# Kernel tuning notes

Measured on AMD Instinct MI355X. Metric: run time of the kernel, lower is better.

The kernel has to match this reference:

```python
import jax, jax.numpy as jnp
import numpy as np

DIM = 192
STATE = 64
B = 8
H = 64
W = 64
EPS_LN = 1e-5
EPS_BN = 1e-5


def _layernorm(x, g, b):
    m = jnp.mean(x, axis=-1, keepdims=True)
    v = jnp.mean((x - m) ** 2, axis=-1, keepdims=True)
    return (x - m) / jnp.sqrt(v + EPS_LN) * g + b


def _linear(x, w, b=None):
    # torch Linear convention: w is [out, in]
    y = jnp.einsum('...i,oi->...o', x, w)
    return y if b is None else y + b


def _parallel_scan(A, Bd, xp):
    # A, Bd, xp: [B, L, S]; h_t = A_t*h_{t-1} + Bd_t*xp_t via log-space cumsum
    A_safe = jnp.clip(A, 0.001, 0.999)
    log_A = jnp.log(A_safe + 1e-10)
    log_cum_A = jnp.cumsum(log_A, axis=1)
    log_cum_A_max = jnp.max(log_cum_A, axis=1, keepdims=True)
    cum_A = jnp.exp(log_cum_A - log_cum_A_max)
    BX = Bd * xp
    # prepend zeros, drop last: normalizer uses cumprod up to t-1
    log_pad = jnp.pad(log_cum_A - log_cum_A_max, ((0, 0), (1, 0), (0, 0)))[:, :-1]
    BX_norm = BX * jnp.exp(-log_pad)
    return jnp.cumsum(BX_norm, axis=1) * cum_A


def _ssm(x, ln_g, ln_b, xp_w, xp_b, dt_w, dt_b, A_log, B_w, C_w, Dp, out_w, out_b):
    xn = _layernorm(x, ln_g, ln_b)
    delta = jax.nn.softplus(_linear(xn, dt_w, dt_b)) * 0.01 + 0.0001  # [B,L,S]
    B_t = _linear(xn, B_w)
    C_t = _linear(xn, C_w)
    A = -jnp.exp(A_log)  # [S]
    x_proj = _linear(xn, xp_w, xp_b)
    deltaA = jnp.clip(delta * A, -10.0, -0.0001)
    A_disc = jnp.exp(deltaA)
    B_disc = delta * B_t
    h = _parallel_scan(A_disc, B_disc, x_proj)
    y = C_t * h
    y = jnp.where(jnp.all(jnp.isfinite(y)), y, jnp.zeros_like(y))
    y = _linear(y, out_w, out_b)
    return y + jnp.clip(Dp, -2.0, 2.0) * x


def reference(x, ln1_g, ln1_b, ln2_g, ln2_b, dw_w, bn_g, bn_b, bn_rm, bn_rv,
              ssm_ln_g, ssm_ln_b, xp_w, xp_b, dt_w, dt_b, A_log, B_w, C_w,
              D_param, out_w, out_b, mlp_w1, mlp_b1, mlp_w2, mlp_b2,
              alpha_local, alpha_ssm, alpha_mlp):
    identity = x
    # depthwise 3x3 conv + BatchNorm2d (eval mode, running stats)
    xc = jax.lax.conv_general_dilated(
        x, dw_w, (1, 1), 'SAME', feature_group_count=DIM,
        dimension_numbers=('NCHW', 'OIHW', 'NCHW'))
    scale = (bn_g / jnp.sqrt(bn_rv + EPS_BN))[None, :, None, None]
    x_local = (xc - bn_rm[None, :, None, None]) * scale + bn_b[None, :, None, None]
    # SSM branch on flattened spatial sequence
    x_seq = x.transpose(0, 2, 3, 1).reshape(B, H * W, DIM)
    x_seq = _layernorm(x_seq, ln1_g, ln1_b)
    x_seq = _ssm(x_seq, ssm_ln_g, ssm_ln_b, xp_w, xp_b, dt_w, dt_b, A_log,
                 B_w, C_w, D_param, out_w, out_b)
    x_ssm = x_seq.reshape(B, H, W, DIM).transpose(0, 3, 1, 2)
    xr = identity + alpha_local * x_local + alpha_ssm * x_ssm
    # residual MLP (dropout = identity at inference)
    x_mlp = xr.transpose(0, 2, 3, 1).reshape(B, H * W, DIM)
    x_mlp = _layernorm(x_mlp, ln2_g, ln2_b)
    x_mlp = _linear(jax.nn.gelu(_linear(x_mlp, mlp_w1, mlp_b1), approximate=False),
                    mlp_w2, mlp_b2)
    return xr + alpha_mlp * x_mlp.reshape(B, H, W, DIM).transpose(0, 3, 1, 2)


def setup_inputs() -> dict:
    key = jax.random.key(0)
    ks = jax.random.split(key, 12)
    def nrm(k, shape, s):
        return jax.random.normal(k, shape, jnp.float32) * s
    f32 = jnp.float32
    return {
        'x': jax.random.normal(ks[0], (B, DIM, H, W), f32),
        'ln1_g': jnp.ones(DIM, f32), 'ln1_b': jnp.zeros(DIM, f32),
        'ln2_g': jnp.ones(DIM, f32), 'ln2_b': jnp.zeros(DIM, f32),
        'dw_w': nrm(ks[1], (DIM, 1, 3, 3), 0.2),
        'bn_g': jnp.ones(DIM, f32), 'bn_b': jnp.zeros(DIM, f32),
        'bn_rm': jnp.zeros(DIM, f32), 'bn_rv': jnp.ones(DIM, f32),
        'ssm_ln_g': jnp.ones(DIM, f32), 'ssm_ln_b': jnp.zeros(DIM, f32),
        'xp_w': nrm(ks[2], (STATE, DIM), 0.05), 'xp_b': jnp.zeros(STATE, f32),
        'dt_w': nrm(ks[3], (STATE, DIM), 0.05), 'dt_b': jnp.zeros(STATE, f32),
        'A_log': jnp.log(jax.random.uniform(ks[4], (STATE,), f32) * 0.8 + 0.2),
        'B_w': nrm(ks[5], (STATE, DIM), 0.05),
        'C_w': nrm(ks[6], (STATE, DIM), 0.05),
        'D_param': jnp.zeros(DIM, f32),
        'out_w': nrm(ks[7], (DIM, STATE), 0.05), 'out_b': jnp.zeros(DIM, f32),
        'mlp_w1': nrm(ks[8], (4 * DIM, DIM), 0.03), 'mlp_b1': jnp.zeros(4 * DIM, f32),
        'mlp_w2': nrm(ks[9], (DIM, 4 * DIM), 0.03), 'mlp_b2': jnp.zeros(DIM, f32),
        'alpha_local': jnp.full((1,), 0.5, f32),
        'alpha_ssm': jnp.full((1,), 0.5, f32),
        'alpha_mlp': jnp.full((1,), 0.5, f32),
    }
```

## Files before the change

### kernel.cpp

```cpp
#include <hip/hip_runtime.h>
#include <hip/hip_bf16.h>
#include <math.h>


#define DEV static __device__ __forceinline__

constexpr int Bn = 8, Dm = 192, Ln = 4096, Sn = 64, Hd = 768;

typedef __attribute__((ext_vector_type(8))) short bf16x8;
typedef __attribute__((ext_vector_type(4))) float f32x4;

DEV short f2b(float x) {
  __hip_bfloat16 h = __float2bfloat16(x);
  return *(short*)&h;
}

DEV float b2f(short x) {
  __hip_bfloat16 h = *(__hip_bfloat16*)&x;
  return __bfloat162float(h);
}

__global__ __launch_bounds__(256) void k_prep(
    const float* __restrict__ x, const float* __restrict__ g1, const float* __restrict__ b1,
    const float* __restrict__ g2, const float* __restrict__ b2,
    short* __restrict__ xnb, short* __restrict__ xln1b,
    const float* __restrict__ dt_w, const float* __restrict__ B_w,
    const float* __restrict__ C_w, const float* __restrict__ xp_w,
    const float* __restrict__ out_w, const float* __restrict__ w1,
    const float* __restrict__ w2, short* __restrict__ wb) {
  __shared__ __align__(16) float tile[Dm * 65];
  int tid = threadIdx.x;
  if (blockIdx.y == 8) {
    for (int i = blockIdx.x * 256 + tid; i < 89088; i += 64 * 256) {
      const float4* src;
      if (i < 3072)       src = (const float4*)dt_w + i;
      else if (i < 6144)  src = (const float4*)B_w + (i - 3072);
      else if (i < 9216)  src = (const float4*)C_w + (i - 6144);
      else if (i < 12288) src = (const float4*)xp_w + (i - 9216);
      else if (i < 15360) src = (const float4*)out_w + (i - 12288);
      else if (i < 52224) src = (const float4*)w1 + (i - 15360);
      else                src = (const float4*)w2 + (i - 52224);
      float4 v = *src;
      int o = i * 4;
      wb[o] = f2b(v.x); wb[o + 1] = f2b(v.y); wb[o + 2] = f2b(v.z); wb[o + 3] = f2b(v.w);
    }
    return;
  }
  int b = blockIdx.y, l0 = blockIdx.x * 64;
  const float* xb = x + (size_t)b * Dm * Ln;
  for (int i = tid; i < Dm * 16; i += 256) {
    int d = i >> 4, l4 = (i & 15) << 2;
    float4 v = *(const float4*)&xb[d * Ln + l0 + l4];
    tile[d * 65 + l4]     = v.x; tile[d * 65 + l4 + 1] = v.y;
    tile[d * 65 + l4 + 2] = v.z; tile[d * 65 + l4 + 3] = v.w;
  }
  __syncthreads();
  int pix = tid >> 2, part = tid & 3, c0 = part * 48;
  float v[48];
  float s1 = 0.f, q1 = 0.f;
#pragma unroll
  for (int j = 0; j < 48; j++) {
    float t = tile[(c0 + j) * 65 + pix];
    v[j] = t; s1 += t; q1 += t * t;
  }
  s1 += __shfl_xor(s1, 1); s1 += __shfl_xor(s1, 2);
  q1 += __shfl_xor(q1, 1); q1 += __shfl_xor(q1, 2);
  float m = s1 * (1.f / 192.f);
  float inv = rsqrtf(q1 * (1.f / 192.f) - m * m + 1e-5f);
  float s2 = 0.f, q2 = 0.f;
#pragma unroll
  for (int j = 0; j < 48; j++) {
    float y = (v[j] - m) * inv * g1[c0 + j] + b1[c0 + j];
    v[j] = y; s2 += y; q2 += y * y;
  }
  s2 += __shfl_xor(s2, 1); s2 += __shfl_xor(s2, 2);
  q2 += __shfl_xor(q2, 1); q2 += __shfl_xor(q2, 2);
  float m2 = s2 * (1.f / 192.f);
  float inv2 = rsqrtf(q2 * (1.f / 192.f) - m2 * m2 + 1e-5f);
  size_t base = ((size_t)b * Ln + l0 + pix) * Dm + c0;
#pragma unroll
  for (int j = 0; j < 48; j += 8) {
    int4 yo, no;
    short* yp = (short*)&yo; short* np = (short*)&no;
#pragma unroll
    for (int k = 0; k < 8; k++) {
      float y = v[j + k];
      yp[k] = f2b(y);
      np[k] = f2b((y - m2) * inv2 * g2[c0 + j + k] + b2[c0 + j + k]);
    }
    *(int4*)&xln1b[base + j] = yo;
    *(int4*)&xnb[base + j]   = no;
  }
}

__global__ __launch_bounds__(256) void k_proj(
    const short* __restrict__ xnb, const short* __restrict__ wcat,
    const float* __restrict__ dt_b, const float* __restrict__ xp_b,
    const float* __restrict__ A_log, float* __restrict__ aA, unsigned* __restrict__ bxc,
    float* __restrict__ sums) {
  __shared__ __align__(16) short As[64 * 72];
  __shared__ __align__(16) short Bs[256 * 72];
  int m0 = blockIdx.x * 64, tid = threadIdx.x;
  int lane = tid & 63, l16 = lane & 15, quad = lane >> 4, w = tid >> 6;
  f32x4 acc[16] = {};
  for (int kt = 0; kt < 3; kt++) {
    int kb = kt * 64;
    for (int i = tid; i < 512; i += 256) {
      int row = i >> 3, c8 = (i & 7) * 8;
      *(float4*)&As[row * 72 + c8] = *(const float4*)&xnb[(size_t)(m0 + row) * 192 + kb + c8];
    }
    for (int i = tid; i < 2048; i += 256) {
      int row = i >> 3, c8 = (i & 7) * 8;
      *(float4*)&Bs[row * 72 + c8] = *(const float4*)&wcat[(size_t)row * 192 + kb + c8];
    }
    __syncthreads();
#pragma unroll
    for (int ks = 0; ks < 2; ks++) {
      int ko = ks * 32 + quad * 8;
      bf16x8 a0 = *(const bf16x8*)&As[(w * 16 + l16) * 72 + ko];
#pragma unroll
      for (int nh = 0; nh < 2; nh++) {
        bf16x8 bfr[8];
#pragma unroll
        for (int j = 0; j < 8; j++) bfr[j] = *(const bf16x8*)&Bs[((nh * 8 + j) * 16 + l16) * 72 + ko];
#pragma unroll
        for (int j = 0; j < 8; j++)
          acc[nh * 8 + j] = __builtin_amdgcn_mfma_f32_16x16x32_bf16(a0, bfr[j], acc[nh * 8 + j], 0, 0, 0);
      }
    }
    __syncthreads();
  }
  float* aAs = (float*)Bs;
  float* bxs = aAs + 64 * 65;
  float Av[4], dtbv[4], xpbv[4];
#pragma unroll
  for (int ni = 0; ni < 4; ni++) {
    int s = ni * 16 + l16;
    Av[ni] = -expf(A_log[s]); dtbv[ni] = dt_b[s]; xpbv[ni] = xp_b[s];
  }
#pragma unroll
  for (int r = 0; r < 4; r++) {
    int lm = w * 16 + quad * 4 + r;
    int m = m0 + lm;
#pragma unroll
    for (int ni = 0; ni < 4; ni++) {
      int s = ni * 16 + l16;
      float z = acc[ni][r] + dtbv[ni];
      float sp = (z > 20.f) ? z : log1pf(expf(z));
      float delta = sp * 0.01f + 0.0001f;
      float bt  = acc[ni + 4][r];
      float ct  = acc[ni + 8][r];
      float xpv = acc[ni + 12][r] + xpbv[ni];
      float dA = fminf(fmaxf(delta * Av[ni], -10.f), -0.0001f);
      float Ae = fminf(fmaxf(expf(dA), 0.001f), 0.999f) + 1e-10f;
      short bxh = f2b(delta * bt * xpv);
      aA[(size_t)m * 64 + s] = Ae;
      unsigned pk = (unsigned)(unsigned short)bxh
                  | ((unsigned)(unsigned short)f2b(ct) << 16);
      bxc[(size_t)m * 64 + s] = pk;
      aAs[lm * 65 + s] = Ae;
      bxs[lm * 65 + s] = b2f(bxh);
    }
  }
  __syncthreads();
  int s = tid & 63, seg = tid >> 6, chunk = seg >> 1, sub = seg & 1;
  bool first = ((m0 & 4095) == 0) && (chunk == 0) && (sub == 0);
  float P = 1.f, H = 0.f;
  int base = chunk * 32 + sub * 16;
#pragma unroll
  for (int j = 0; j < 16; j++) {
    float a  = aAs[(base + j) * 65 + s];
    float bx = bxs[(base + j) * 65 + s];
    if (first && j == 0) { P = a; H = bx; }
    else { P *= a; H = a * (H + bx); }
  }
  float* partP = (float*)As;
  float* partH = partP + 256;
  partP[seg * 64 + s] = P; partH[seg * 64 + s] = H;
  __syncthreads();
  if (tid < 128) {
    int c = tid >> 6;
    float p0 = partP[(c * 2) * 64 + s], p1 = partP[(c * 2 + 1) * 64 + s];
    float h0 = partH[(c * 2) * 64 + s], h1 = partH[(c * 2 + 1) * 64 + s];
    int ci = (m0 >> 12) * 128 + ((m0 & 4095) >> 5) + c;
    sums[(ci * 2 + 0) * 64 + s] = p0 * p1;
    sums[(ci * 2 + 1) * 64 + s] = p1 * h0 + h1;
  }
}

__global__ __launch_bounds__(256) void k_conv(
    const float* __restrict__ x, const float* __restrict__ dw,
    const float* __restrict__ bn_g, const float* __restrict__ bn_b,
    const float* __restrict__ bn_rm, const float* __restrict__ bn_rv,
    const float* __restrict__ a_loc, float* __restrict__ xr,
    const float* __restrict__ sums, float* __restrict__ carries) {
  __shared__ __align__(16) float xs[64 * 64];
  int tid = threadIdx.x;
  if (blockIdx.x == 192) {
    float* Pp = xs;
    float* Hp = xs + 256;
    int b = blockIdx.y, s = tid & 63, q = tid >> 6;
    float P = 1.f, H = 0.f;
#pragma unroll 4
    for (int j = 0; j < 32; j++) {
      int ci = b * 128 + q * 32 + j;
      float a = sums[(ci * 2 + 0) * 64 + s];
      float h = sums[(ci * 2 + 1) * 64 + s];
      P *= a; H = a * H + h;
    }
    Pp[q * 64 + s] = P; Hp[q * 64 + s] = H;
    __syncthreads();
    float cur = 0.f;
    for (int qq = 0; qq < q; qq++) cur = Pp[qq * 64 + s] * cur + Hp[qq * 64 + s];
#pragma unroll 4
    for (int j = 0; j < 32; j++) {
      int ci = b * 128 + q * 32 + j;
      carries[ci * 64 + s] = cur;
      float a = sums[(ci * 2 + 0) * 64 + s];
      float h = sums[(ci * 2 + 1) * 64 + s];
      cur = a * cur + h;
    }
    return;
  }
  int d = blockIdx.x, b = blockIdx.y;
  const float* xp = x + ((size_t)b * Dm + d) * Ln;
  for (int i = tid; i < 1024; i += 256) ((float4*)xs)[i] = ((const float4*)xp)[i];
  __syncthreads();
  float w[9];
#pragma unroll
  for (int k = 0; k < 9; k++) w[k] = dw[d * 9 + k];
  float scale = bn_g[d] * rsqrtf(bn_rv[d] + 1e-5f);
  float rm = bn_rm[d], bb = bn_b[d];
  float al = a_loc[0];
  float* xo = xr + ((size_t)b * Dm + d) * Ln;
  for (int i = tid; i < 4096; i += 256) {
    int h = i >> 6, wc = i & 63;
    float acc = 0.f;
#pragma unroll
    for (int kh = 0; kh < 3; kh++) {
      int hh = h + kh - 1;
      if (hh < 0 || hh >= 64) continue;
#pragma unroll
      for (int kw = 0; kw < 3; kw++) {
        int ww2 = wc + kw - 1;
        if (ww2 < 0 || ww2 >= 64) continue;
        acc += xs[hh * 64 + ww2] * w[kh * 3 + kw];
      }
    }
    float xl = (acc - rm) * scale + bb;
    xo[i] = xs[i] + al * xl;
  }
}

__global__ __launch_bounds__(256) void k_out(
    const float* __restrict__ aA, const unsigned* __restrict__ bxc,
    const float* __restrict__ carries,
    const short* __restrict__ owb, const float* __restrict__ out_b,
    const float* __restrict__ Dp, const short* __restrict__ xln1b,
    const float* __restrict__ a_ssm, const float* __restrict__ g2,
    const float* __restrict__ bb2,
    float* __restrict__ xr, short* __restrict__ xn2) {
  __shared__ __align__(16) float smemf[64 * 193];
  short* As = (short*)smemf;
  short* Bs = (short*)smemf + 192 * 72;
  float* tile = smemf;
  int l0g = blockIdx.x * 64, tid = threadIdx.x;
  int lane = tid & 63, l16 = lane & 15, quad = lane >> 4, wv = tid >> 6;
  for (int i = tid; i < 1536; i += 256) {
    int row = i >> 3, c8 = (i & 7) * 8;
    *(float4*)&As[row * 72 + c8] = *(const float4*)&owb[row * 64 + c8];
  }
  int bb = l0g >> 12, c0 = (l0g & 4095) >> 5;
  float xrv[3][4][4];
#pragma unroll
  for (int mi = 0; mi < 3; mi++)
#pragma unroll
    for (int r = 0; r < 4; r++) {
      int d = wv * 48 + mi * 16 + quad * 4 + r;
#pragma unroll
      for (int ni = 0; ni < 4; ni++) {
        int l = l0g + ni * 16 + l16;
        xrv[mi][r][ni] = xr[((size_t)bb * Dm + d) * Ln + (l & 4095)];
      }
    }
  if (wv < 2) {
    int c = c0 + wv, s = lane;
    float h = carries[(bb * 128 + c) * 64 + s];
    const float* ap = aA + (size_t)(l0g + wv * 32) * 64;
    const unsigned* bp = bxc + (size_t)(l0g + wv * 32) * 64;
    int t = 0;
    if (c == 0) {
      unsigned u = bp[s];
      h = b2f((short)(u & 0xFFFF));
      Bs[(wv * 32) * 72 + s] = f2b(b2f((short)(u >> 16)) * h);
      t = 1;
    }
#pragma unroll 4
    for (; t < 32; t++) {
      unsigned u = bp[t * 64 + s];
      float a = ap[t * 64 + s];
      h = a * (h + b2f((short)(u & 0xFFFF)));
      Bs[(wv * 32 + t) * 72 + s] = f2b(b2f((short)(u >> 16)) * h);
    }
  }
  __syncthreads();
  f32x4 acc[3][4] = {};
#pragma unroll
  for (int ks = 0; ks < 2; ks++) {
    int ko = ks * 32 + quad * 8;
    bf16x8 a[3], b[4];
#pragma unroll
    for (int mi = 0; mi < 3; mi++) a[mi] = *(const bf16x8*)&As[(wv * 48 + mi * 16 + l16) * 72 + ko];
#pragma unroll
    for (int ni = 0; ni < 4; ni++) b[ni] = *(const bf16x8*)&Bs[(ni * 16 + l16) * 72 + ko];
#pragma unroll
    for (int mi = 0; mi < 3; mi++)
#pragma unroll
      for (int ni = 0; ni < 4; ni++)
        acc[mi][ni] = __builtin_amdgcn_mfma_f32_16x16x32_bf16(a[mi], b[ni], acc[mi][ni], 0, 0, 0);
  }
  __syncthreads();
  float as_ = a_ssm[0];
#pragma unroll
  for (int mi = 0; mi < 3; mi++)
#pragma unroll
    for (int r = 0; r < 4; r++) {
      int d = wv * 48 + mi * 16 + quad * 4 + r;
      float ob = out_b[d];
      float dc = fminf(fmaxf(Dp[d], -2.f), 2.f);
#pragma unroll
      for (int ni = 0; ni < 4; ni++) {
        int l = l0g + ni * 16 + l16;
        float v = acc[mi][ni][r] + ob;
        if (dc != 0.f) v += dc * b2f(xln1b[(size_t)l * 192 + d]);
        size_t idx = ((size_t)bb * Dm + d) * Ln + (l & 4095);
        float nx = xrv[mi][r][ni] + as_ * v;
        xr[idx] = nx;
        tile[(l & 63) * 193 + d] = nx;
      }
    }
  __syncthreads();
  int pix = tid >> 2, part = tid & 3, c0p = part * 48;
  float vv[48];
  float s1 = 0.f, q1 = 0.f;
#pragma unroll
  for (int j = 0; j < 48; j++) {
    float t = tile[pix * 193 + c0p + j];
    vv[j] = t; s1 += t; q1 += t * t;
  }
  s1 += __shfl_xor(s1, 1); s1 += __shfl_xor(s1, 2);
  q1 += __shfl_xor(q1, 1); q1 += __shfl_xor(q1, 2);
  float m = s1 * (1.f / 192.f);
  float inv = rsqrtf(q1 * (1.f / 192.f) - m * m + 1e-5f);
  size_t obase = (size_t)(l0g + pix) * Dm + c0p;
#pragma unroll
  for (int j = 0; j < 48; j += 8) {
    int4 no; short* np = (short*)&no;
#pragma unroll
    for (int k = 0; k < 8; k++)
      np[k] = f2b((vv[j + k] - m) * inv * g2[c0p + j + k] + bb2[c0p + j + k]);
    *(int4*)&xn2[obase + j] = no;
  }
}

__global__ __launch_bounds__(256) void k_gemm1(
    const short* __restrict__ xn2, const short* __restrict__ w1b,
    const float* __restrict__ b1h, short* __restrict__ hid) {
  __shared__ __align__(16) short smem[128 * 72 + 64 * 72];
  short* As = smem;
  short* Bs = smem + 128 * 72;
  int bid = blockIdx.x;
  int xcd = bid & 7, p = bid >> 3;
  int m0 = (xcd * 32 + p / 12) * 128, n0 = (p % 12) * 64;
  int tid = threadIdx.x;
  int lane = tid & 63, l16 = lane & 15, quad = lane >> 4;
  int wm = (tid >> 6) >> 1, wn = (tid >> 6) & 1;
  f32x4 acc[4][2] = {};
  for (int kt = 0; kt < 3; kt++) {
    int kb = kt * 64;
    for (int i = tid; i < 1024; i += 256) {
      int row = i >> 3, c8 = (i & 7) * 8;
      *(float4*)&As[row * 72 + c8] = *(const float4*)&xn2[(size_t)(m0 + row) * 192 + kb + c8];
    }
    for (int i = tid; i < 512; i += 256) {
      int row = i >> 3, c8 = (i & 7) * 8;
      *(float4*)&Bs[row * 72 + c8] = *(const float4*)&w1b[(size_t)(n0 + row) * 192 + kb + c8];
    }
    __syncthreads();
#pragma unroll
    for (int ks = 0; ks < 2; ks++) {
      int ko = ks * 32 + quad * 8;
      bf16x8 a[4], b[2];
#pragma unroll
      for (int mi = 0; mi < 4; mi++) a[mi] = *(const bf16x8*)&As[(wm * 64 + mi * 16 + l16) * 72 + ko];
#pragma unroll
      for (int ni = 0; ni < 2; ni++) b[ni] = *(const bf16x8*)&Bs[(wn * 32 + ni * 16 + l16) * 72 + ko];
#pragma unroll
      for (int mi = 0; mi < 4; mi++)
#pragma unroll
        for (int ni = 0; ni < 2; ni++)
          acc[mi][ni] = __builtin_amdgcn_mfma_f32_16x16x32_bf16(a[mi], b[ni], acc[mi][ni], 0, 0, 0);
    }
    __syncthreads();
  }
  short* Cs = smem;
  float bias2[2];
#pragma unroll
  for (int ni = 0; ni < 2; ni++) bias2[ni] = b1h[n0 + wn * 32 + ni * 16 + l16];
#pragma unroll
  for (int mi = 0; mi < 4; mi++)
#pragma unroll
    for (int ni = 0; ni < 2; ni++) {
      int n = wn * 32 + ni * 16 + l16;
#pragma unroll
      for (int r = 0; r < 4; r++) {
        int m = wm * 64 + mi * 16 + quad * 4 + r;
        float v = acc[mi][ni][r] + bias2[ni];
        float g = 0.5f * v * (1.f + erff(v * 0.70710678118f));
        Cs[m * 72 + n] = f2b(g);
      }
    }
  __syncthreads();
  for (int i = tid; i < 1024; i += 256) {
    int m = i >> 3, ch = i & 7;
    *(float4*)&hid[(size_t)(m0 + m) * 768 + n0 + ch * 8] = *(const float4*)&Cs[m * 72 + ch * 8];
  }
}

__global__ __launch_bounds__(256) void k_gemm2(
    const short* __restrict__ hid, const short* __restrict__ w2b,
    const float* __restrict__ b2o, const float* __restrict__ xr,
    const float* __restrict__ am, float* __restrict__ out) {
  __shared__ __align__(16) short Wt[96 * 72];
  __shared__ __align__(16) short Ht[64 * 72];
  int bid = blockIdx.x;
  int xcd = bid & 7, p = bid >> 3;
  int l0g = (xcd * 64 + (p >> 1)) * 64, d0 = (p & 1) * 96;
  int tid = threadIdx.x;
  int lane = tid & 63, l16 = lane & 15, quad = lane >> 4;
  int wm = (tid >> 6) >> 1, wn = (tid >> 6) & 1;
  f32x4 acc[3][2] = {};
  for (int kt = 0; kt < 12; kt++) {
    int kb = kt * 64;
    for (int i = tid; i < 768; i += 256) {
      int row = i >> 3, c8 = (i & 7) * 8;
      *(float4*)&Wt[row * 72 + c8] = *(const float4*)&w2b[(size_t)(d0 + row) * 768 + kb + c8];
    }
    for (int i = tid; i < 512; i += 256) {
      int row = i >> 3, c8 = (i & 7) * 8;
      *(float4*)&Ht[row * 72 + c8] = *(const float4*)&hid[(size_t)(l0g + row) * 768 + kb + c8];
    }
    __syncthreads();
#pragma unroll
    for (int ks = 0; ks < 2; ks++) {
      int ko = ks * 32 + quad * 8;
      bf16x8 a[3], b[2];
#pragma unroll
      for (int mi = 0; mi < 3; mi++) a[mi] = *(const bf16x8*)&Wt[(wm * 48 + mi * 16 + l16) * 72 + ko];
#pragma unroll
      for (int ni = 0; ni < 2; ni++) b[ni] = *(const bf16x8*)&Ht[(wn * 32 + ni * 16 + l16) * 72 + ko];
#pragma unroll
      for (int mi = 0; mi < 3; mi++)
#pragma unroll
        for (int ni = 0; ni < 2; ni++)
          acc[mi][ni] = __builtin_amdgcn_mfma_f32_16x16x32_bf16(a[mi], b[ni], acc[mi][ni], 0, 0, 0);
    }
    __syncthreads();
  }
  float alpha = am[0];
#pragma unroll
  for (int mi = 0; mi < 3; mi++)
#pragma unroll
    for (int r = 0; r < 4; r++) {
      int d = d0 + wm * 48 + mi * 16 + quad * 4 + r;
      float bias = b2o[d];
#pragma unroll
      for (int ni = 0; ni < 2; ni++) {
        int lg = l0g + wn * 32 + ni * 16 + l16;
        size_t idx = ((size_t)(lg >> 12) * Dm + d) * Ln + (lg & 4095);
        out[idx] = xr[idx] + alpha * (acc[mi][ni][r] + bias);
      }
    }
}

extern "C" void kernel_launch(void* const* d_in, const int* in_sizes, int n_in,
                              void* d_out, int out_size, void* d_ws, size_t ws_size,
                              hipStream_t stream) {
  (void)in_sizes; (void)n_in; (void)out_size; (void)ws_size;
  const float* x     = (const float*)d_in[0];
  const float* ln1_g = (const float*)d_in[1];
  const float* ln1_b = (const float*)d_in[2];
  const float* ln2_g = (const float*)d_in[3];
  const float* ln2_b = (const float*)d_in[4];
  const float* dw_w  = (const float*)d_in[5];
  const float* bn_g  = (const float*)d_in[6];
  const float* bn_b  = (const float*)d_in[7];
  const float* bn_rm = (const float*)d_in[8];
  const float* bn_rv = (const float*)d_in[9];
  const float* ssm_g = (const float*)d_in[10];
  const float* ssm_b = (const float*)d_in[11];
  const float* xp_w  = (const float*)d_in[12];
  const float* xp_b  = (const float*)d_in[13];
  const float* dt_w  = (const float*)d_in[14];
  const float* dt_b  = (const float*)d_in[15];
  const float* A_log = (const float*)d_in[16];
  const float* B_w   = (const float*)d_in[17];
  const float* C_w   = (const float*)d_in[18];
  const float* Dp    = (const float*)d_in[19];
  const float* out_w = (const float*)d_in[20];
  const float* out_b = (const float*)d_in[21];
  const float* w1    = (const float*)d_in[22];
  const float* b1    = (const float*)d_in[23];
  const float* w2    = (const float*)d_in[24];
  const float* b2    = (const float*)d_in[25];
  const float* a_loc = (const float*)d_in[26];
  const float* a_ssm = (const float*)d_in[27];
  const float* a_mlp = (const float*)d_in[28];

  float* ws = (float*)d_ws;
  short*    xnb   = (short*)ws;
  short*    xln1b = (short*)(ws + 3145728);
  float*    aA    = ws + 6291456;
  unsigned* bxc   = (unsigned*)(ws + 8388608);
  float*    xr    = ws + 17825792;
  short*    wb    = (short*)(ws + 24117248);
  float*    sums  = ws + 24829952;
  float*    carr  = ws + 24961024;
  short*    xn2   = (short*)(ws + 25026560);
  short*    hid   = (short*)(ws + 28172288);
  short*    wcatb = wb;
  short*    owb   = wb + 49152;
  short*    w1b   = wb + 61440;
  short*    w2b   = wb + 208896;
  float*    out   = (float*)d_out;

  k_prep <<<dim3(64, 9),  256, 0, stream>>>(x, ln1_g, ln1_b, ssm_g, ssm_b, xnb, xln1b,
                                            dt_w, B_w, C_w, xp_w, out_w, w1, w2, wb);
  k_proj <<<dim3(512),    256, 0, stream>>>(xnb, wcatb, dt_b, xp_b, A_log, aA, bxc, sums);
  k_conv <<<dim3(193, 8), 256, 0, stream>>>(x, dw_w, bn_g, bn_b, bn_rm, bn_rv, a_loc, xr,
                                            sums, carr);
  k_out  <<<dim3(512),    256, 0, stream>>>(aA, bxc, carr, owb, out_b, Dp, xln1b,
                                            a_ssm, ln2_g, ln2_b, xr, xn2);
  k_gemm1<<<dim3(3072),   256, 0, stream>>>(xn2, w1b, b1, hid);
  k_gemm2<<<dim3(1024),   256, 0, stream>>>(hid, w2b, b2, xr, a_mlp, out);
}
```

Measured before the change: 262.5 us.

## Merge conv into projection kernel and recompute scan carries in output kernel

The depthwise conv/BN blocks are now extra blocks of the projection kernel, which removes one launch and lets conv work overlap with the projection GEMM. The cross-chunk carry scan that used to run in the conv kernel is moved into k_out. Each output block recomputes its own prefix carries from the chunk sums, so the carries buffer and the serial dependency through conv go away. The cost is redundant prefix work in every k_out block, up to 128 sequential chunk combines per wave, plus two extra block barriers.

```diff
diff --git a/kernel.cpp b/kernel.cpp
--- a/kernel.cpp
+++ b/kernel.cpp
@@ -93,14 +93,53 @@
   }
 }
 
-__global__ __launch_bounds__(256) void k_proj(
+__global__ __launch_bounds__(256) void k_projconv(
     const short* __restrict__ xnb, const short* __restrict__ wcat,
     const float* __restrict__ dt_b, const float* __restrict__ xp_b,
     const float* __restrict__ A_log, float* __restrict__ aA, unsigned* __restrict__ bxc,
-    float* __restrict__ sums) {
-  __shared__ __align__(16) short As[64 * 72];
-  __shared__ __align__(16) short Bs[256 * 72];
-  int m0 = blockIdx.x * 64, tid = threadIdx.x;
+    float* __restrict__ sums,
+    const float* __restrict__ x, const float* __restrict__ dw,
+    const float* __restrict__ bn_g, const float* __restrict__ bn_b,
+    const float* __restrict__ bn_rm, const float* __restrict__ bn_rv,
+    const float* __restrict__ a_loc, float* __restrict__ xr) {
+  __shared__ __align__(16) short smem[64 * 72 + 256 * 72];
+  int tid = threadIdx.x;
+  if (blockIdx.x >= 512) {
+    float* xs = (float*)smem;
+    int i6 = blockIdx.x - 512;
+    int d = i6 % 192, b = i6 / 192;
+    const float* xp = x + ((size_t)b * Dm + d) * Ln;
+    for (int i = tid; i < 1024; i += 256) ((float4*)xs)[i] = ((const float4*)xp)[i];
+    __syncthreads();
+    float w[9];
+#pragma unroll
+    for (int k = 0; k < 9; k++) w[k] = dw[d * 9 + k];
+    float scale = bn_g[d] * rsqrtf(bn_rv[d] + 1e-5f);
+    float rm = bn_rm[d], bb = bn_b[d];
+    float al = a_loc[0];
+    float* xo = xr + ((size_t)b * Dm + d) * Ln;
+    for (int i = tid; i < 4096; i += 256) {
+      int h = i >> 6, wc = i & 63;
+      float acc = 0.f;
+#pragma unroll
+      for (int kh = 0; kh < 3; kh++) {
+        int hh = h + kh - 1;
+        if (hh < 0 || hh >= 64) continue;
+#pragma unroll
+        for (int kw = 0; kw < 3; kw++) {
+          int ww2 = wc + kw - 1;
+          if (ww2 < 0 || ww2 >= 64) continue;
+          acc += xs[hh * 64 + ww2] * w[kh * 3 + kw];
+        }
+      }
+      float xl = (acc - rm) * scale + bb;
+      xo[i] = xs[i] + al * xl;
+    }
+    return;
+  }
+  short* As = smem;
+  short* Bs = smem + 64 * 72;
+  int m0 = blockIdx.x * 64;
   int lane = tid & 63, l16 = lane & 15, quad = lane >> 4, w = tid >> 6;
   f32x4 acc[16] = {};
   for (int kt = 0; kt < 3; kt++) {
@@ -188,73 +227,9 @@
   }
 }
 
-__global__ __launch_bounds__(256) void k_conv(
-    const float* __restrict__ x, const float* __restrict__ dw,
-    const float* __restrict__ bn_g, const float* __restrict__ bn_b,
-    const float* __restrict__ bn_rm, const float* __restrict__ bn_rv,
-    const float* __restrict__ a_loc, float* __restrict__ xr,
-    const float* __restrict__ sums, float* __restrict__ carries) {
-  __shared__ __align__(16) float xs[64 * 64];
-  int tid = threadIdx.x;
-  if (blockIdx.x == 192) {
-    float* Pp = xs;
-    float* Hp = xs + 256;
-    int b = blockIdx.y, s = tid & 63, q = tid >> 6;
-    float P = 1.f, H = 0.f;
-#pragma unroll 4
-    for (int j = 0; j < 32; j++) {
-      int ci = b * 128 + q * 32 + j;
-      float a = sums[(ci * 2 + 0) * 64 + s];
-      float h = sums[(ci * 2 + 1) * 64 + s];
-      P *= a; H = a * H + h;
-    }
-    Pp[q * 64 + s] = P; Hp[q * 64 + s] = H;
-    __syncthreads();
-    float cur = 0.f;
-    for (int qq = 0; qq < q; qq++) cur = Pp[qq * 64 + s] * cur + Hp[qq * 64 + s];
-#pragma unroll 4
-    for (int j = 0; j < 32; j++) {
-      int ci = b * 128 + q * 32 + j;
-      carries[ci * 64 + s] = cur;
-      float a = sums[(ci * 2 + 0) * 64 + s];
-      float h = sums[(ci * 2 + 1) * 64 + s];
-      cur = a * cur + h;
-    }
-    return;
-  }
-  int d = blockIdx.x, b = blockIdx.y;
-  const float* xp = x + ((size_t)b * Dm + d) * Ln;
-  for (int i = tid; i < 1024; i += 256) ((float4*)xs)[i] = ((const float4*)xp)[i];
-  __syncthreads();
-  float w[9];
-#pragma unroll
-  for (int k = 0; k < 9; k++) w[k] = dw[d * 9 + k];
-  float scale = bn_g[d] * rsqrtf(bn_rv[d] + 1e-5f);
-  float rm = bn_rm[d], bb = bn_b[d];
-  float al = a_loc[0];
-  float* xo = xr + ((size_t)b * Dm + d) * Ln;
-  for (int i = tid; i < 4096; i += 256) {
-    int h = i >> 6, wc = i & 63;
-    float acc = 0.f;
-#pragma unroll
-    for (int kh = 0; kh < 3; kh++) {
-      int hh = h + kh - 1;
-      if (hh < 0 || hh >= 64) continue;
-#pragma unroll
-      for (int kw = 0; kw < 3; kw++) {
-        int ww2 = wc + kw - 1;
-        if (ww2 < 0 || ww2 >= 64) continue;
-        acc += xs[hh * 64 + ww2] * w[kh * 3 + kw];
-      }
-    }
-    float xl = (acc - rm) * scale + bb;
-    xo[i] = xs[i] + al * xl;
-  }
-}
-
 __global__ __launch_bounds__(256) void k_out(
     const float* __restrict__ aA, const unsigned* __restrict__ bxc,
-    const float* __restrict__ carries,
+    const float* __restrict__ sums,
     const short* __restrict__ owb, const float* __restrict__ out_b,
     const float* __restrict__ Dp, const short* __restrict__ xln1b,
     const float* __restrict__ a_ssm, const float* __restrict__ g2,
@@ -263,6 +238,9 @@
   __shared__ __align__(16) float smemf[64 * 193];
   short* As = (short*)smemf;
   short* Bs = (short*)smemf + 192 * 72;
+  float* Pp   = smemf + 9216;
+  float* Hp   = Pp + 256;
+  float* cbuf = Hp + 256;
   float* tile = smemf;
   int l0g = blockIdx.x * 64, tid = threadIdx.x;
   int lane = tid & 63, l16 = lane & 15, quad = lane >> 4, wv = tid >> 6;
@@ -283,9 +261,35 @@
         xrv[mi][r][ni] = xr[((size_t)bb * Dm + d) * Ln + (l & 4095)];
       }
     }
+  int qstar = c0 >> 5, jstar = c0 & 31;
+  float Pj0 = 1.f, Hj0 = 0.f, Pj1 = 1.f, Hj1 = 0.f;
+  {
+    int q = wv, s = lane;
+    if (q <= qstar) {
+      float P = 1.f, H = 0.f;
+      int nj = (q == qstar) ? (jstar + 2) : 32;
+      for (int j = 0; j < nj; j++) {
+        if (q == qstar && j == jstar)     { Pj0 = P; Hj0 = H; }
+        if (q == qstar && j == jstar + 1) { Pj1 = P; Hj1 = H; }
+        int ci = bb * 128 + q * 32 + j;
+        float a = sums[(ci * 2 + 0) * 64 + s];
+        float h = sums[(ci * 2 + 1) * 64 + s];
+        P *= a; H = a * H + h;
+      }
+      if (q < qstar) { Pp[q * 64 + s] = P; Hp[q * 64 + s] = H; }
+    }
+  }
+  __syncthreads();
+  if (wv == qstar) {
+    float C = 0.f;
+    for (int qq = 0; qq < qstar; qq++) C = Pp[qq * 64 + lane] * C + Hp[qq * 64 + lane];
+    cbuf[lane]      = Pj0 * C + Hj0;
+    cbuf[64 + lane] = Pj1 * C + Hj1;
+  }
+  __syncthreads();
   if (wv < 2) {
     int c = c0 + wv, s = lane;
-    float h = carries[(bb * 128 + c) * 64 + s];
+    float h = cbuf[wv * 64 + s];
     const float* ap = aA + (size_t)(l0g + wv * 32) * 64;
     const unsigned* bp = bxc + (size_t)(l0g + wv * 32) * 64;
     int t = 0;
@@ -525,7 +529,6 @@
   float*    xr    = ws + 17825792;
   short*    wb    = (short*)(ws + 24117248);
   float*    sums  = ws + 24829952;
-  float*    carr  = ws + 24961024;
   short*    xn2   = (short*)(ws + 25026560);
   short*    hid   = (short*)(ws + 28172288);
   short*    wcatb = wb;
@@ -534,13 +537,12 @@
   short*    w2b   = wb + 208896;
   float*    out   = (float*)d_out;
 
-  k_prep <<<dim3(64, 9),  256, 0, stream>>>(x, ln1_g, ln1_b, ssm_g, ssm_b, xnb, xln1b,
-                                            dt_w, B_w, C_w, xp_w, out_w, w1, w2, wb);
-  k_proj <<<dim3(512),    256, 0, stream>>>(xnb, wcatb, dt_b, xp_b, A_log, aA, bxc, sums);
-  k_conv <<<dim3(193, 8), 256, 0, stream>>>(x, dw_w, bn_g, bn_b, bn_rm, bn_rv, a_loc, xr,
-                                            sums, carr);
-  k_out  <<<dim3(512),    256, 0, stream>>>(aA, bxc, carr, owb, out_b, Dp, xln1b,
-                                            a_ssm, ln2_g, ln2_b, xr, xn2);
-  k_gemm1<<<dim3(3072),   256, 0, stream>>>(xn2, w1b, b1, hid);
-  k_gemm2<<<dim3(1024),   256, 0, stream>>>(hid, w2b, b2, xr, a_mlp, out);
-}
+  k_prep    <<<dim3(64, 9), 256, 0, stream>>>(x, ln1_g, ln1_b, ssm_g, ssm_b, xnb, xln1b,
+                                              dt_w, B_w, C_w, xp_w, out_w, w1, w2, wb);
+  k_projconv<<<dim3(2048),  256, 0, stream>>>(xnb, wcatb, dt_b, xp_b, A_log, aA, bxc, sums,
+                                              x, dw_w, bn_g, bn_b, bn_rm, bn_rv, a_loc, xr);
+  k_out     <<<dim3(512),   256, 0, stream>>>(aA, bxc, sums, owb, out_b, Dp, xln1b,
+                                              a_ssm, ln2_g, ln2_b, xr, xn2);
+  k_gemm1   <<<dim3(3072),  256, 0, stream>>>(xn2, w1b, b1, hid);
+  k_gemm2   <<<dim3(1024),  256, 0, stream>>>(hid, w2b, b2, xr, a_mlp, out);
+}
```

After: 278.1 us. +5.9%, slower.

## Fuse layernorm prep into SSM projection GEMM and use tanh GELU approximation

Applied to the files above, without the earlier changes.

Splits weight conversion into its own kernel and fuses the double layernorm into the projection GEMM, so the normalized SSM input stays in shared memory instead of round-tripping through a global bf16 buffer. Shared memory per block grows (a 192x65 float tile reused for the B tiles plus a wider A tile), which may reduce occupancy. Separately replaces exact erf GELU with the tanh approximation using fast exp, a small numerical deviation from the reference.

```diff
diff --git a/kernel.cpp b/kernel.cpp
--- a/kernel.cpp
+++ b/kernel.cpp
@@ -20,33 +20,40 @@
   return __bfloat162float(h);
 }
 
-__global__ __launch_bounds__(256) void k_prep(
-    const float* __restrict__ x, const float* __restrict__ g1, const float* __restrict__ b1,
-    const float* __restrict__ g2, const float* __restrict__ b2,
-    short* __restrict__ xnb, short* __restrict__ xln1b,
+__global__ __launch_bounds__(256) void k_weights(
     const float* __restrict__ dt_w, const float* __restrict__ B_w,
     const float* __restrict__ C_w, const float* __restrict__ xp_w,
     const float* __restrict__ out_w, const float* __restrict__ w1,
     const float* __restrict__ w2, short* __restrict__ wb) {
-  __shared__ __align__(16) float tile[Dm * 65];
-  int tid = threadIdx.x;
-  if (blockIdx.y == 8) {
-    for (int i = blockIdx.x * 256 + tid; i < 89088; i += 64 * 256) {
-      const float4* src;
-      if (i < 3072)       src = (const float4*)dt_w + i;
-      else if (i < 6144)  src = (const float4*)B_w + (i - 3072);
-      else if (i < 9216)  src = (const float4*)C_w + (i - 6144);
-      else if (i < 12288) src = (const float4*)xp_w + (i - 9216);
-      else if (i < 15360) src = (const float4*)out_w + (i - 12288);
-      else if (i < 52224) src = (const float4*)w1 + (i - 15360);
-      else                src = (const float4*)w2 + (i - 52224);
-      float4 v = *src;
-      int o = i * 4;
-      wb[o] = f2b(v.x); wb[o + 1] = f2b(v.y); wb[o + 2] = f2b(v.z); wb[o + 3] = f2b(v.w);
-    }
-    return;
-  }
-  int b = blockIdx.y, l0 = blockIdx.x * 64;
+  for (int i = blockIdx.x * 256 + threadIdx.x; i < 89088; i += 64 * 256) {
+    const float4* src;
+    if (i < 3072)       src = (const float4*)dt_w + i;
+    else if (i < 6144)  src = (const float4*)B_w + (i - 3072);
+    else if (i < 9216)  src = (const float4*)C_w + (i - 6144);
+    else if (i < 12288) src = (const float4*)xp_w + (i - 9216);
+    else if (i < 15360) src = (const float4*)out_w + (i - 12288);
+    else if (i < 52224) src = (const float4*)w1 + (i - 15360);
+    else                src = (const float4*)w2 + (i - 52224);
+    float4 v = *src;
+    int o = i * 4;
+    wb[o] = f2b(v.x); wb[o + 1] = f2b(v.y); wb[o + 2] = f2b(v.z); wb[o + 3] = f2b(v.w);
+  }
+}
+
+__global__ __launch_bounds__(256) void k_fproj(
+    const float* __restrict__ x,
+    const float* __restrict__ g1, const float* __restrict__ b1,
+    const float* __restrict__ g2, const float* __restrict__ b2,
+    short* __restrict__ xln1b,
+    const short* __restrict__ wcat,
+    const float* __restrict__ dt_b, const float* __restrict__ xp_b,
+    const float* __restrict__ A_log, float* __restrict__ aA, unsigned* __restrict__ bxc,
+    float* __restrict__ sums) {
+  __shared__ __align__(16) short As[64 * 200];
+  __shared__ __align__(16) float uni[192 * 65];
+  int m0 = blockIdx.x * 64, tid = threadIdx.x;
+  int b = m0 >> 12, l0 = m0 & 4095;
+  float* tile = uni;
   const float* xb = x + (size_t)b * Dm * Ln;
   for (int i = tid; i < Dm * 16; i += 256) {
     int d = i >> 4, l4 = (i & 15) << 2;
@@ -55,60 +62,50 @@
     tile[d * 65 + l4 + 2] = v.z; tile[d * 65 + l4 + 3] = v.w;
   }
   __syncthreads();
-  int pix = tid >> 2, part = tid & 3, c0 = part * 48;
-  float v[48];
-  float s1 = 0.f, q1 = 0.f;
-#pragma unroll
-  for (int j = 0; j < 48; j++) {
-    float t = tile[(c0 + j) * 65 + pix];
-    v[j] = t; s1 += t; q1 += t * t;
-  }
-  s1 += __shfl_xor(s1, 1); s1 += __shfl_xor(s1, 2);
-  q1 += __shfl_xor(q1, 1); q1 += __shfl_xor(q1, 2);
-  float m = s1 * (1.f / 192.f);
-  float inv = rsqrtf(q1 * (1.f / 192.f) - m * m + 1e-5f);
-  float s2 = 0.f, q2 = 0.f;
-#pragma unroll
-  for (int j = 0; j < 48; j++) {
-    float y = (v[j] - m) * inv * g1[c0 + j] + b1[c0 + j];
-    v[j] = y; s2 += y; q2 += y * y;
-  }
-  s2 += __shfl_xor(s2, 1); s2 += __shfl_xor(s2, 2);
-  q2 += __shfl_xor(q2, 1); q2 += __shfl_xor(q2, 2);
-  float m2 = s2 * (1.f / 192.f);
-  float inv2 = rsqrtf(q2 * (1.f / 192.f) - m2 * m2 + 1e-5f);
-  size_t base = ((size_t)b * Ln + l0 + pix) * Dm + c0;
-#pragma unroll
-  for (int j = 0; j < 48; j += 8) {
-    int4 yo, no;
-    short* yp = (short*)&yo; short* np = (short*)&no;
-#pragma unroll
-    for (int k = 0; k < 8; k++) {
-      float y = v[j + k];
-      yp[k] = f2b(y);
-      np[k] = f2b((y - m2) * inv2 * g2[c0 + j + k] + b2[c0 + j + k]);
-    }
-    *(int4*)&xln1b[base + j] = yo;
-    *(int4*)&xnb[base + j]   = no;
-  }
-}
-
-__global__ __launch_bounds__(256) void k_proj(
-    const short* __restrict__ xnb, const short* __restrict__ wcat,
-    const float* __restrict__ dt_b, const float* __restrict__ xp_b,
-    const float* __restrict__ A_log, float* __restrict__ aA, unsigned* __restrict__ bxc,
-    float* __restrict__ sums) {
-  __shared__ __align__(16) short As[64 * 72];
-  __shared__ __align__(16) short Bs[256 * 72];
-  int m0 = blockIdx.x * 64, tid = threadIdx.x;
+  {
+    int pix = tid >> 2, part = tid & 3, c0 = part * 48;
+    float v[48];
+    float s1 = 0.f, q1 = 0.f;
+#pragma unroll
+    for (int j = 0; j < 48; j++) {
+      float t = tile[(c0 + j) * 65 + pix];
+      v[j] = t; s1 += t; q1 += t * t;
+    }
+    s1 += __shfl_xor(s1, 1); s1 += __shfl_xor(s1, 2);
+    q1 += __shfl_xor(q1, 1); q1 += __shfl_xor(q1, 2);
+    float m = s1 * (1.f / 192.f);
+    float inv = rsqrtf(q1 * (1.f / 192.f) - m * m + 1e-5f);
+    float s2 = 0.f, q2 = 0.f;
+#pragma unroll
+    for (int j = 0; j < 48; j++) {
+      float y = (v[j] - m) * inv * g1[c0 + j] + b1[c0 + j];
+      v[j] = y; s2 += y; q2 += y * y;
+    }
+    s2 += __shfl_xor(s2, 1); s2 += __shfl_xor(s2, 2);
+    q2 += __shfl_xor(q2, 1); q2 += __shfl_xor(q2, 2);
+    float m2 = s2 * (1.f / 192.f);
+    float inv2 = rsqrtf(q2 * (1.f / 192.f) - m2 * m2 + 1e-5f);
+    size_t base = (size_t)(m0 + pix) * Dm + c0;
+#pragma unroll
+    for (int j = 0; j < 48; j += 8) {
+      int4 yo, no;
+      short* yp = (short*)&yo; short* np = (short*)&no;
+#pragma unroll
+      for (int k = 0; k < 8; k++) {
+        float y = v[j + k];
+        yp[k] = f2b(y);
+        np[k] = f2b((y - m2) * inv2 * g2[c0 + j + k] + b2[c0 + j + k]);
+      }
+      *(int4*)&xln1b[base + j] = yo;
+      *(int4*)&As[pix * 200 + c0 + j] = no;
+    }
+  }
+  __syncthreads();
+  short* Bs = (short*)uni;
   int lane = tid & 63, l16 = lane & 15, quad = lane >> 4, w = tid >> 6;
   f32x4 acc[16] = {};
   for (int kt = 0; kt < 3; kt++) {
     int kb = kt * 64;
-    for (int i = tid; i < 512; i += 256) {
-      int row = i >> 3, c8 = (i & 7) * 8;
-      *(float4*)&As[row * 72 + c8] = *(const float4*)&xnb[(size_t)(m0 + row) * 192 + kb + c8];
-    }
     for (int i = tid; i < 2048; i += 256) {
       int row = i >> 3, c8 = (i & 7) * 8;
       *(float4*)&Bs[row * 72 + c8] = *(const float4*)&wcat[(size_t)row * 192 + kb + c8];
@@ -117,7 +114,7 @@
 #pragma unroll
     for (int ks = 0; ks < 2; ks++) {
       int ko = ks * 32 + quad * 8;
-      bf16x8 a0 = *(const bf16x8*)&As[(w * 16 + l16) * 72 + ko];
+      bf16x8 a0 = *(const bf16x8*)&As[(w * 16 + l16) * 200 + kb + ko];
 #pragma unroll
       for (int nh = 0; nh < 2; nh++) {
         bf16x8 bfr[8];
@@ -130,7 +127,7 @@
     }
     __syncthreads();
   }
-  float* aAs = (float*)Bs;
+  float* aAs = uni;
   float* bxs = aAs + 64 * 65;
   float Av[4], dtbv[4], xpbv[4];
 #pragma unroll
@@ -416,7 +413,9 @@
       for (int r = 0; r < 4; r++) {
         int m = wm * 64 + mi * 16 + quad * 4 + r;
         float v = acc[mi][ni][r] + bias2[ni];
-        float g = 0.5f * v * (1.f + erff(v * 0.70710678118f));
+        float u = 0.7978845608f * (v + 0.044715f * v * v * v);
+        float e = __expf(2.f * u);
+        float g = 0.5f * v * (1.f + (e - 1.f) / (e + 1.f));
         Cs[m * 72 + n] = f2b(g);
       }
     }
@@ -518,7 +517,6 @@
   const float* a_mlp = (const float*)d_in[28];
 
   float* ws = (float*)d_ws;
-  short*    xnb   = (short*)ws;
   short*    xln1b = (short*)(ws + 3145728);
   float*    aA    = ws + 6291456;
   unsigned* bxc   = (unsigned*)(ws + 8388608);
@@ -534,13 +532,13 @@
   short*    w2b   = wb + 208896;
   float*    out   = (float*)d_out;
 
-  k_prep <<<dim3(64, 9),  256, 0, stream>>>(x, ln1_g, ln1_b, ssm_g, ssm_b, xnb, xln1b,
-                                            dt_w, B_w, C_w, xp_w, out_w, w1, w2, wb);
-  k_proj <<<dim3(512),    256, 0, stream>>>(xnb, wcatb, dt_b, xp_b, A_log, aA, bxc, sums);
-  k_conv <<<dim3(193, 8), 256, 0, stream>>>(x, dw_w, bn_g, bn_b, bn_rm, bn_rv, a_loc, xr,
-                                            sums, carr);
-  k_out  <<<dim3(512),    256, 0, stream>>>(aA, bxc, carr, owb, out_b, Dp, xln1b,
-                                            a_ssm, ln2_g, ln2_b, xr, xn2);
-  k_gemm1<<<dim3(3072),   256, 0, stream>>>(xn2, w1b, b1, hid);
-  k_gemm2<<<dim3(1024),   256, 0, stream>>>(hid, w2b, b2, xr, a_mlp, out);
-}
+  k_weights<<<dim3(64),     256, 0, stream>>>(dt_w, B_w, C_w, xp_w, out_w, w1, w2, wb);
+  k_fproj  <<<dim3(512),    256, 0, stream>>>(x, ln1_g, ln1_b, ssm_g, ssm_b, xln1b,
+                                              wcatb, dt_b, xp_b, A_log, aA, bxc, sums);
+  k_conv   <<<dim3(193, 8), 256, 0, stream>>>(x, dw_w, bn_g, bn_b, bn_rm, bn_rv, a_loc, xr,
+                                              sums, carr);
+  k_out    <<<dim3(512),    256, 0, stream>>>(aA, bxc, carr, owb, out_b, Dp, xln1b,
+                                              a_ssm, ln2_g, ln2_b, xr, xn2);
+  k_gemm1  <<<dim3(3072),   256, 0, stream>>>(xn2, w1b, b1, hid);
+  k_gemm2  <<<dim3(1024),   256, 0, stream>>>(hid, w2b, b2, xr, a_mlp, out);
+}
```

Result: no change. 264.8 us (+0.9%).
